# Performance work log

Hardware: AMD Instinct MI355X
Metric: run time of the kernel (lower is better)

## Reference

```python
import jax, jax.numpy as jnp
import numpy as np

N_NODES = 100000
N_EDGES = 1600000
N_GRAPHS = 64
NEG_SLOPE = 0.2


def gat_conv(x, W, att_src, att_dst, bias, edge_index, n_nodes, heads, out_ch, concat):
    """PyG-style GATConv (eval mode, self loops already included in edge_index)."""
    h = (x @ W).reshape(n_nodes, heads, out_ch)            # [N, H, C]
    a_src = jnp.einsum('nhc,hc->nh', h, att_src)           # [N, H]
    a_dst = jnp.einsum('nhc,hc->nh', h, att_dst)           # [N, H]
    src, dst = edge_index[0], edge_index[1]
    e = jax.nn.leaky_relu(a_src[src] + a_dst[dst], NEG_SLOPE)   # [E, H]
    # segment softmax over incoming edges of each destination node
    m = jax.ops.segment_max(e, dst, num_segments=n_nodes)      # [N, H]
    ex = jnp.exp(e - m[dst])
    denom = jax.ops.segment_sum(ex, dst, num_segments=n_nodes) # [N, H]
    alpha = ex / denom[dst]                                     # [E, H]
    msg = h[src] * alpha[:, :, None]                            # [E, H, C]
    out = jax.ops.segment_sum(msg, dst, num_segments=n_nodes)   # [N, H, C]
    if concat:
        out = out.reshape(n_nodes, heads * out_ch)
    else:
        out = out.mean(axis=1)
    return out + bias


def setup_inputs() -> dict:
    key = jax.random.key(0)
    ks = jax.random.split(key, 16)
    x = jax.random.normal(ks[0], (N_NODES, 1), dtype=jnp.float32)
    edge_index = jax.random.randint(ks[1], (2, N_EDGES), 0, N_NODES, dtype=jnp.int64)
    batch = jnp.sort(jax.random.randint(ks[2], (N_NODES,), 0, N_GRAPHS, dtype=jnp.int64))
    def glorot(k, shape):
        fan = (shape[0] + shape[-1])
        return jax.random.uniform(k, shape, jnp.float32, -1.0, 1.0) * np.sqrt(6.0 / fan)
    # layer 1: in=1, heads=8, out=8, concat
    W1 = glorot(ks[3], (1, 64))
    att_src1 = glorot(ks[4], (8, 8))
    att_dst1 = glorot(ks[5], (8, 8))
    b1 = jnp.zeros((64,), jnp.float32)
    # layer 2: in=64, heads=8, out=16, mean
    W2 = glorot(ks[6], (64, 128))
    att_src2 = glorot(ks[7], (8, 16))
    att_dst2 = glorot(ks[8], (8, 16))
    b2 = jnp.zeros((16,), jnp.float32)
    # fc 16 -> 4
    Wfc = glorot(ks[9], (16, 4))
    bfc = jnp.zeros((4,), jnp.float32)
    return dict(x=x, W1=W1, att_src1=att_src1, att_dst1=att_dst1, b1=b1,
                W2=W2, att_src2=att_src2, att_dst2=att_dst2, b2=b2,
                Wfc=Wfc, bfc=bfc, edge_index=edge_index, batch=batch)


def reference(x, W1, att_src1, att_dst1, b1, W2, att_src2, att_dst2, b2, Wfc, bfc, edge_index, batch):
    n = x.shape[0]
    # PyG GATConv default add_self_loops=True
    loops = jnp.arange(n, dtype=edge_index.dtype)
    ei = jnp.concatenate([edge_index, jnp.stack([loops, loops])], axis=1)
    h = gat_conv(x, W1, att_src1, att_dst1, b1, ei, n, heads=8, out_ch=8, concat=True)
    h = jax.nn.elu(h)
    # F.dropout(training=False) and attention dropout are no-ops in eval mode
    h = gat_conv(h, W2, att_src2, att_dst2, b2, ei, n, heads=8, out_ch=16, concat=False)
    # global mean pool over graphs
    sums = jax.ops.segment_sum(h, batch, num_segments=N_GRAPHS)          # [G, 16]
    cnts = jax.ops.segment_sum(jnp.ones((n,), h.dtype), batch, num_segments=N_GRAPHS)
    pooled = sums / jnp.maximum(cnts, 1.0)[:, None]
    return pooled @ Wfc + bfc                                            # [G, 4]
```

## Files before the change

### kernel.cpp

```cpp
#include <hip/hip_runtime.h>
#include <hip/hip_fp16.h>

#define N_NODES  100000
#define N_EDGES  1600000
#define N_GRAPHS 64

#define BINSH  9
#define NBIN   196
#define BINCAP 16384
#define EPB    4096

__device__ __forceinline__ float lrelu(float v) { return v > 0.f ? v : 0.2f * v; }
__device__ __forceinline__ float elu_f(float v) { return v > 0.f ? v : __expf(v) - 1.f; }
__device__ __forceinline__ float rdlane_f(float v, int lane) {
    return __int_as_float(__builtin_amdgcn_readlane(__float_as_int(v), lane));
}

__global__ __launch_bounds__(256) void k_binA(
    const int* __restrict__ src, const int* __restrict__ dst,
    const int* __restrict__ batch, int* __restrict__ gbin_cursor,
    int* __restrict__ cnt, int2* __restrict__ binned) {
    __shared__ int hist[NBIN], lexcl[NBIN], runbase[NBIN], lcur[NBIN];
    __shared__ int scan[256];
    __shared__ int gh[N_GRAPHS];
    __shared__ int2 stage[EPB];
    int t = threadIdx.x;
    int e0 = blockIdx.x * EPB;
    for (int b = t; b < NBIN; b += 256) hist[b] = 0;
    if (t < N_GRAPHS) gh[t] = 0;
    __syncthreads();
    int nid = blockIdx.x * 256 + t;
    if (nid < N_NODES) atomicAdd(&gh[batch[nid]], 1);
    for (int i = t; i < EPB; i += 256) {
        int e = e0 + i;
        if (e < N_EDGES) atomicAdd(&hist[dst[e] >> BINSH], 1);
    }
    __syncthreads();
    int v = (t < NBIN) ? hist[t] : 0;
    scan[t] = v;
    __syncthreads();
    for (int d = 1; d < 256; d <<= 1) {
        int a = (t >= d) ? scan[t - d] : 0;
        __syncthreads();
        scan[t] += a;
        __syncthreads();
    }
    if (t < NBIN) { lexcl[t] = scan[t] - v; lcur[t] = scan[t] - v; }
    __syncthreads();
    if (t < NBIN && hist[t] > 0) runbase[t] = atomicAdd(&gbin_cursor[t], hist[t]);
    if (t < N_GRAPHS && gh[t]) atomicAdd(&cnt[t], gh[t]);
    __syncthreads();
    for (int i = t; i < EPB; i += 256) {
        int e = e0 + i;
        if (e < N_EDGES) {
            int d = dst[e];
            int b = d >> BINSH;
            int p = atomicAdd(&lcur[b], 1);
            stage[p] = make_int2(src[e], d);
        }
    }
    __syncthreads();
    int m = N_EDGES - e0;
    if (m > EPB) m = EPB;
    for (int i = t; i < m; i += 256) {
        int2 pr = stage[i];
        int b = pr.y >> BINSH;
        binned[(size_t)b * BINCAP + runbase[b] + (i - lexcl[b])] = pr;
    }
}

__global__ void k_binscan(const int* __restrict__ gbin_cursor, int* __restrict__ bin_base) {
    __shared__ int sm[256];
    int t = threadIdx.x;
    int v = (t < NBIN) ? gbin_cursor[t] : 0;
    sm[t] = v;
    __syncthreads();
    for (int d = 1; d < 256; d <<= 1) {
        int a = (t >= d) ? sm[t - d] : 0;
        __syncthreads();
        sm[t] += a;
        __syncthreads();
    }
    if (t < NBIN) bin_base[t] = sm[t] - v;
    if (t == 0) bin_base[NBIN] = N_EDGES;
}

__global__ __launch_bounds__(1024) void k_binB(
    const int2* __restrict__ binned, const int* __restrict__ gbin_cursor,
    const int* __restrict__ bin_base, int* __restrict__ off, int* __restrict__ csr) {
    __shared__ int hist[512], sc[512];
    int b = blockIdx.x, t = threadIdx.x;
    int count = gbin_cursor[b];
    int ebase = bin_base[b];
    int node0 = b << BINSH;
    const int2* my = binned + (size_t)b * BINCAP;
    if (t < 512) hist[t] = 0;
    __syncthreads();
    for (int i = t; i < count; i += 1024) atomicAdd(&hist[my[i].y - node0], 1);
    __syncthreads();
    int v = (t < 512) ? hist[t] : 0;
    if (t < 512) sc[t] = v;
    __syncthreads();
    for (int d = 1; d < 512; d <<= 1) {
        int a = (t < 512 && t >= d) ? sc[t - d] : 0;
        __syncthreads();
        if (t < 512) sc[t] += a;
        __syncthreads();
    }
    if (t < 512) {
        int n = node0 + t;
        if (n < N_NODES) off[n] = ebase + sc[t] - v;
        hist[t] = sc[t] - v;
    }
    if (b == 0 && t == 0) off[N_NODES] = N_EDGES;
    __syncthreads();
    for (int i = t; i < count; i += 1024) {
        int2 pr = my[i];
        int p = atomicAdd(&hist[pr.y - node0], 1);
        csr[ebase + p] = pr.x;
    }
}

__global__ __launch_bounds__(256) void k_l1gemm(
    const float* __restrict__ x, const float* __restrict__ W1,
    const float* __restrict__ as1, const float* __restrict__ ad1,
    const float* __restrict__ b1, const float* __restrict__ W2,
    const float* __restrict__ as2, const float* __restrict__ ad2,
    const int* __restrict__ off, const int* __restrict__ csr,
    __half2* __restrict__ h2p, float2* __restrict__ ap, float2* __restrict__ dp) {
    __shared__ float4 smW4[32 * 64];
    __shared__ float smS1[16][8];
    __shared__ float smws[8], smwd[8];
    int t = threadIdx.x;
    for (int idx = t; idx < 2048; idx += 256) {
        int k2 = idx >> 6, ll = idx & 63;
        smW4[idx] = make_float4(W2[(2 * k2) * 128 + ll], W2[(2 * k2) * 128 + 64 + ll],
                                W2[(2 * k2 + 1) * 128 + ll], W2[(2 * k2 + 1) * 128 + 64 + ll]);
    }
    if (t < 8) {
        float s = 0.f, d = 0.f;
        for (int c = 0; c < 8; ++c) {
            float w = W1[t * 8 + c];
            s += w * as1[t * 8 + c];
            d += w * ad1[t * 8 + c];
        }
        smws[t] = s;
        smwd[t] = d;
    }
    __syncthreads();

    {
        int nl = t >> 4, c = t & 15;
        int n = blockIdx.x * 16 + nl;
        float ws[8], wd[8];
#pragma unroll
        for (int h = 0; h < 8; ++h) { ws[h] = smws[h]; wd[h] = smwd[h]; }
        float xn = x[n];
        float num[8], den[8];
#pragma unroll
        for (int h = 0; h < 8; ++h) { num[h] = 0.f; den[h] = 0.f; }
        if (c == 0) {
#pragma unroll
            for (int h = 0; h < 8; ++h) {
                float w = __expf(lrelu(xn * ws[h] + xn * wd[h]));
                den[h] = w;
                num[h] = w * xn;
            }
        }
        int b = off[n], e = off[n + 1];
        for (int i = b + c; i < e; i += 16) {
            int s = csr[i];
            float xs = x[s];
#pragma unroll
            for (int h = 0; h < 8; ++h) {
                float w = __expf(lrelu(xs * ws[h] + xn * wd[h]));
                den[h] += w;
                num[h] += w * xs;
            }
        }
#pragma unroll
        for (int d = 1; d < 16; d <<= 1) {
#pragma unroll
            for (int h = 0; h < 8; ++h) {
                num[h] += __shfl_xor(num[h], d, 64);
                den[h] += __shfl_xor(den[h], d, 64);
            }
        }
        if (c == 0) {
#pragma unroll
            for (int h = 0; h < 8; ++h) smS1[nl][h] = num[h] / den[h];
        }
    }
    __syncthreads();

    int wid = t >> 6, l = t & 63;
    float w1l = W1[l], b1l = b1[l];
    float asA = as2[l], asB = as2[64 + l], adA = ad2[l], adB = ad2[64 + l];
    for (int q = 0; q < 4; ++q) {
        int nl = wid * 4 + q;
        int n = blockIdx.x * 16 + nl;
        float a = elu_f(smS1[nl][l >> 3] * w1l + b1l);
        float acc0 = 0.f, acc1 = 0.f;
#pragma unroll
        for (int k2 = 0; k2 < 32; ++k2) {
            float4 wv = smW4[k2 * 64 + l];
            float a0 = rdlane_f(a, 2 * k2);
            float a1 = rdlane_f(a, 2 * k2 + 1);
            acc0 += a0 * wv.x + a1 * wv.z;
            acc1 += a0 * wv.y + a1 * wv.w;
        }
        h2p[n * 64 + l] = __floats2half2_rn(acc0, acc1);

        float pSA = acc0 * asA;
        float pSB = acc1 * asB;
        float pDA = acc0 * adA;
        float pDB = acc1 * adB;
#pragma unroll
        for (int d = 1; d < 16; d <<= 1) {
            pSA += __shfl_xor(pSA, d, 64);
            pSB += __shfl_xor(pSB, d, 64);
            pDA += __shfl_xor(pDA, d, 64);
            pDB += __shfl_xor(pDB, d, 64);
        }
        if ((l & 15) == 0) {
            int h = l >> 4;
            ap[n * 4 + h] = make_float2(pSA, pSB);
            dp[n * 4 + h] = make_float2(pDA, pDB);
        }
    }
}

__global__ __launch_bounds__(256) void k_layer2(
    const __half2* __restrict__ h2p, const float2* __restrict__ ap,
    const float2* __restrict__ dp, const int* __restrict__ off,
    const int* __restrict__ csr, const int* __restrict__ batch,
    float* __restrict__ pool) {
    __shared__ float smv[4][16];
    __shared__ int smg[4];
    const float* apf = (const float*)ap;
    const float* dpf = (const float*)dp;
    int t = threadIdx.x;
    int wid = t >> 6, l = t & 63;
    int n = blockIdx.x * 4 + wid;
    int hA = l >> 4;
    int hh = l & 7;
    int j8 = l >> 3;
    int fidx = 2 * (hh & 3) + (hh >> 2);
    float dn = dpf[n * 8 + fidx];

    float2 ad = dp[n * 4 + hA];
    float2 an = ap[n * 4 + hA];
    float wA = __expf(lrelu(an.x + ad.x));
    float wB = __expf(lrelu(an.y + ad.y));
    float2 hn = __half22float2(h2p[n * 64 + l]);
    float accA = wA * hn.x, accB = wB * hn.y;
    float denTA = wA, denTB = wB;
    float wsum = 0.f;

    int b = off[n];
    int deg = off[n + 1] - b;
    for (int base = 0; base < deg; base += 64) {
        int rem = deg - base;
        if (rem > 64) rem = 64;
        int sl = (l < rem) ? csr[b + base + l] : 0;
        int g = 0;
        for (; g + 8 <= rem; g += 8) {
            int sg = __shfl(sl, g + j8, 64);
            float w = __expf(lrelu(apf[sg * 8 + fidx] + dn));
            wsum += w;
#pragma unroll
            for (int j2 = 0; j2 < 8; ++j2) {
                int s = __builtin_amdgcn_readlane(sl, g + j2);
                float wa = __shfl(w, j2 * 8 + hA, 64);
                float wb = __shfl(w, j2 * 8 + hA + 4, 64);
                float2 gg = __half22float2(h2p[s * 64 + l]);
                accA = fmaf(wa, gg.x, accA);
                accB = fmaf(wb, gg.y, accB);
            }
        }
        if (g < rem) {
            int cnt = rem - g;
            int jj = (j8 < cnt) ? j8 : 0;
            int sg = __shfl(sl, g + jj, 64);
            float w = (j8 < cnt) ? __expf(lrelu(apf[sg * 8 + fidx] + dn)) : 0.f;
            wsum += w;
            for (int j2 = 0; j2 < cnt; ++j2) {
                int s = __builtin_amdgcn_readlane(sl, g + j2);
                float wa = __shfl(w, j2 * 8 + hA, 64);
                float wb = __shfl(w, j2 * 8 + hA + 4, 64);
                float2 gg = __half22float2(h2p[s * 64 + l]);
                accA = fmaf(wa, gg.x, accA);
                accB = fmaf(wb, gg.y, accB);
            }
        }
    }
    wsum += __shfl_xor(wsum, 8, 64);
    wsum += __shfl_xor(wsum, 16, 64);
    wsum += __shfl_xor(wsum, 32, 64);
    float denA = denTA + __shfl(wsum, hA, 64);
    float denB = denTB + __shfl(wsum, hA + 4, 64);

    float v = accA / denA + accB / denB;
    v += __shfl_xor(v, 16, 64);
    v += __shfl_xor(v, 32, 64);
    v *= 0.125f;
    if (l < 16) smv[wid][l] = v;
    if (l == 0) smg[wid] = batch[n];
    __syncthreads();
    if (t < 64) {
        int w = t >> 4, c = t & 15;
        int g = smg[w];
        bool leader = true;
        for (int w2 = 0; w2 < w; ++w2)
            if (smg[w2] == g) { leader = false; break; }
        if (leader) {
            float s = smv[w][c];
            for (int w2 = w + 1; w2 < 4; ++w2)
                if (smg[w2] == g) s += smv[w2][c];
            atomicAdd(&pool[g * 16 + c], s);
        }
    }
}

__global__ void k_final(const float* __restrict__ pool, const int* __restrict__ cnt,
                        const float* __restrict__ b2, const float* __restrict__ Wfc,
                        const float* __restrict__ bfc, float* __restrict__ out) {
    int t = threadIdx.x;
    int g = t >> 2, k = t & 3;
    float c = (float)(cnt[g] > 0 ? cnt[g] : 1);
    float acc = bfc[k];
#pragma unroll
    for (int ci = 0; ci < 16; ++ci)
        acc += (pool[g * 16 + ci] / c + b2[ci]) * Wfc[ci * 4 + k];
    out[g * 4 + k] = acc;
}

extern "C" void kernel_launch(void* const* d_in, const int* in_sizes, int n_in,
                              void* d_out, int out_size, void* d_ws, size_t ws_size,
                              hipStream_t stream) {
    const float* x   = (const float*)d_in[0];
    const float* W1  = (const float*)d_in[1];
    const float* as1 = (const float*)d_in[2];
    const float* ad1 = (const float*)d_in[3];
    const float* b1  = (const float*)d_in[4];
    const float* W2  = (const float*)d_in[5];
    const float* as2 = (const float*)d_in[6];
    const float* ad2 = (const float*)d_in[7];
    const float* b2  = (const float*)d_in[8];
    const float* Wfc = (const float*)d_in[9];
    const float* bfc = (const float*)d_in[10];
    const int* ei    = (const int*)d_in[11];
    const int* batch = (const int*)d_in[12];
    const int* srcv  = ei;
    const int* dstv  = ei + N_EDGES;

    char* ws = (char*)d_ws;
    size_t o = 0;
    auto alloc = [&](size_t bytes) {
        void* p = ws + o;
        o += (bytes + 255) & ~(size_t)255;
        return p;
    };
    int*    cnt     = (int*)alloc(64 * 4);
    float*  pool    = (float*)alloc(64 * 16 * 4);
    int*    gbin    = (int*)alloc(NBIN * 4);
    size_t  zbytes  = o;
    int*    bin_base= (int*)alloc((NBIN + 1) * 4);
    int*    off     = (int*)alloc((size_t)(N_NODES + 1) * 4);
    int*    csr     = (int*)alloc((size_t)N_EDGES * 4);
    char*   ubase   = (char*)alloc((size_t)N_NODES * 64 * 4 + (size_t)N_NODES * 4 * 8 * 2);
    int2*   binned  = (int2*)ubase;
    __half2* h2p    = (__half2*)ubase;
    float2* ap      = (float2*)(ubase + (size_t)N_NODES * 64 * 4);
    float2* dp      = (float2*)(ubase + (size_t)N_NODES * 64 * 4 + (size_t)N_NODES * 4 * 8);

    hipMemsetAsync(d_ws, 0, zbytes, stream);

    int nbA = (N_EDGES + EPB - 1) / EPB;

    k_binA<<<nbA, 256, 0, stream>>>(srcv, dstv, batch, gbin, cnt, binned);
    k_binscan<<<1, 256, 0, stream>>>(gbin, bin_base);
    k_binB<<<NBIN, 1024, 0, stream>>>(binned, gbin, bin_base, off, csr);
    k_l1gemm<<<N_NODES / 16, 256, 0, stream>>>(x, W1, as1, ad1, b1, W2, as2, ad2,
                                               off, csr, h2p, ap, dp);
    k_layer2<<<N_NODES / 4, 256, 0, stream>>>(h2p, ap, dp, off, csr, batch, pool);
    k_final<<<1, 256, 0, stream>>>(pool, cnt, b2, Wfc, bfc, (float*)d_out);
}
```

Before: 319.0 us.

## Split each layer-2 node's edge list across two wavefronts and merge via shared memory

The layer-2 aggregation kernel now assigns two wavefronts to each destination node. Each wave processes alternating 8-edge groups, and the partial accumulators and weight sums are combined through shared memory before normalization and pooling. This shortens each wave's serial gather chain and doubles the memory-level parallelism per node, which matters at an average degree of about 17. In exchange it adds a block barrier, shared-memory traffic, doubled grid size and duplicated per-node setup loads.

```diff
diff --git a/kernel.cpp b/kernel.cpp
--- a/kernel.cpp
+++ b/kernel.cpp
@@ -235,27 +235,35 @@
     const float2* __restrict__ dp, const int* __restrict__ off,
     const int* __restrict__ csr, const int* __restrict__ batch,
     float* __restrict__ pool) {
-    __shared__ float smv[4][16];
-    __shared__ int smg[4];
+    __shared__ float2 smacc[2][64];
+    __shared__ float smw[2][64];
+    __shared__ float smv[2][16];
+    __shared__ int smg[2];
     const float* apf = (const float*)ap;
     const float* dpf = (const float*)dp;
     int t = threadIdx.x;
     int wid = t >> 6, l = t & 63;
-    int n = blockIdx.x * 4 + wid;
+    int nl = wid >> 1, sub = wid & 1;
+    int n = blockIdx.x * 2 + nl;
     int hA = l >> 4;
     int hh = l & 7;
     int j8 = l >> 3;
     int fidx = 2 * (hh & 3) + (hh >> 2);
     float dn = dpf[n * 8 + fidx];
 
+    float accA = 0.f, accB = 0.f, wsum = 0.f;
+    float denTA = 0.f, denTB = 0.f;
     float2 ad = dp[n * 4 + hA];
-    float2 an = ap[n * 4 + hA];
-    float wA = __expf(lrelu(an.x + ad.x));
-    float wB = __expf(lrelu(an.y + ad.y));
-    float2 hn = __half22float2(h2p[n * 64 + l]);
-    float accA = wA * hn.x, accB = wB * hn.y;
-    float denTA = wA, denTB = wB;
-    float wsum = 0.f;
+    if (sub == 0) {
+        float2 an = ap[n * 4 + hA];
+        float wA = __expf(lrelu(an.x + ad.x));
+        float wB = __expf(lrelu(an.y + ad.y));
+        float2 hn = __half22float2(h2p[n * 64 + l]);
+        accA = wA * hn.x;
+        accB = wB * hn.y;
+        denTA = wA;
+        denTB = wB;
+    }
 
     int b = off[n];
     int deg = off[n + 1] - b;
@@ -263,60 +271,68 @@
         int rem = deg - base;
         if (rem > 64) rem = 64;
         int sl = (l < rem) ? csr[b + base + l] : 0;
-        int g = 0;
-        for (; g + 8 <= rem; g += 8) {
-            int sg = __shfl(sl, g + j8, 64);
-            float w = __expf(lrelu(apf[sg * 8 + fidx] + dn));
-            wsum += w;
-#pragma unroll
-            for (int j2 = 0; j2 < 8; ++j2) {
-                int s = __builtin_amdgcn_readlane(sl, g + j2);
-                float wa = __shfl(w, j2 * 8 + hA, 64);
-                float wb = __shfl(w, j2 * 8 + hA + 4, 64);
-                float2 gg = __half22float2(h2p[s * 64 + l]);
-                accA = fmaf(wa, gg.x, accA);
-                accB = fmaf(wb, gg.y, accB);
+        int ng = (rem + 7) >> 3;
+        for (int g8 = sub; g8 < ng; g8 += 2) {
+            int g = g8 * 8;
+            int cnt = rem - g;
+            if (cnt >= 8) {
+                int sg = __shfl(sl, g + j8, 64);
+                float w = __expf(lrelu(apf[sg * 8 + fidx] + dn));
+                wsum += w;
+#pragma unroll
+                for (int j2 = 0; j2 < 8; ++j2) {
+                    int s = __builtin_amdgcn_readlane(sl, g + j2);
+                    float wa = __shfl(w, j2 * 8 + hA, 64);
+                    float wb = __shfl(w, j2 * 8 + hA + 4, 64);
+                    float2 gg = __half22float2(h2p[s * 64 + l]);
+                    accA = fmaf(wa, gg.x, accA);
+                    accB = fmaf(wb, gg.y, accB);
+                }
+            } else {
+                int jj = (j8 < cnt) ? j8 : 0;
+                int sg = __shfl(sl, g + jj, 64);
+                float w = (j8 < cnt) ? __expf(lrelu(apf[sg * 8 + fidx] + dn)) : 0.f;
+                wsum += w;
+                for (int j2 = 0; j2 < cnt; ++j2) {
+                    int s = __builtin_amdgcn_readlane(sl, g + j2);
+                    float wa = __shfl(w, j2 * 8 + hA, 64);
+                    float wb = __shfl(w, j2 * 8 + hA + 4, 64);
+                    float2 gg = __half22float2(h2p[s * 64 + l]);
+                    accA = fmaf(wa, gg.x, accA);
+                    accB = fmaf(wb, gg.y, accB);
+                }
             }
         }
-        if (g < rem) {
-            int cnt = rem - g;
-            int jj = (j8 < cnt) ? j8 : 0;
-            int sg = __shfl(sl, g + jj, 64);
-            float w = (j8 < cnt) ? __expf(lrelu(apf[sg * 8 + fidx] + dn)) : 0.f;
-            wsum += w;
-            for (int j2 = 0; j2 < cnt; ++j2) {
-                int s = __builtin_amdgcn_readlane(sl, g + j2);
-                float wa = __shfl(w, j2 * 8 + hA, 64);
-                float wb = __shfl(w, j2 * 8 + hA + 4, 64);
-                float2 gg = __half22float2(h2p[s * 64 + l]);
-                accA = fmaf(wa, gg.x, accA);
-                accB = fmaf(wb, gg.y, accB);
-            }
-        }
-    }
-    wsum += __shfl_xor(wsum, 8, 64);
-    wsum += __shfl_xor(wsum, 16, 64);
-    wsum += __shfl_xor(wsum, 32, 64);
-    float denA = denTA + __shfl(wsum, hA, 64);
-    float denB = denTB + __shfl(wsum, hA + 4, 64);
-
-    float v = accA / denA + accB / denB;
-    v += __shfl_xor(v, 16, 64);
-    v += __shfl_xor(v, 32, 64);
-    v *= 0.125f;
-    if (l < 16) smv[wid][l] = v;
-    if (l == 0) smg[wid] = batch[n];
-    __syncthreads();
-    if (t < 64) {
+    }
+    if (sub == 1) {
+        smacc[nl][l] = make_float2(accA, accB);
+        smw[nl][l] = wsum;
+    }
+    __syncthreads();
+    if (sub == 0) {
+        float2 o = smacc[nl][l];
+        accA += o.x;
+        accB += o.y;
+        wsum += smw[nl][l];
+        wsum += __shfl_xor(wsum, 8, 64);
+        wsum += __shfl_xor(wsum, 16, 64);
+        wsum += __shfl_xor(wsum, 32, 64);
+        float denA = denTA + __shfl(wsum, hA, 64);
+        float denB = denTB + __shfl(wsum, hA + 4, 64);
+        float v = accA / denA + accB / denB;
+        v += __shfl_xor(v, 16, 64);
+        v += __shfl_xor(v, 32, 64);
+        v *= 0.125f;
+        if (l < 16) smv[nl][l] = v;
+        if (l == 0) smg[nl] = batch[n];
+    }
+    __syncthreads();
+    if (t < 32) {
         int w = t >> 4, c = t & 15;
         int g = smg[w];
-        bool leader = true;
-        for (int w2 = 0; w2 < w; ++w2)
-            if (smg[w2] == g) { leader = false; break; }
-        if (leader) {
+        if (w == 0 || smg[0] != g) {
             float s = smv[w][c];
-            for (int w2 = w + 1; w2 < 4; ++w2)
-                if (smg[w2] == g) s += smv[w2][c];
+            if (w == 0 && smg[1] == g) s += smv[1][c];
             atomicAdd(&pool[g * 16 + c], s);
         }
     }
@@ -383,6 +399,6 @@
     k_binB<<<NBIN, 1024, 0, stream>>>(binned, gbin, bin_base, off, csr);
     k_l1gemm<<<N_NODES / 16, 256, 0, stream>>>(x, W1, as1, ad1, b1, W2, as2, ad2,
                                                off, csr, h2p, ap, dp);
-    k_layer2<<<N_NODES / 4, 256, 0, stream>>>(h2p, ap, dp, off, csr, batch, pool);
+    k_layer2<<<N_NODES / 2, 256, 0, stream>>>(h2p, ap, dp, off, csr, batch, pool);
     k_final<<<1, 256, 0, stream>>>(pool, cnt, b2, Wfc, bfc, (float*)d_out);
 }
```

Result: slower. 372.3 us (+16.7%).

## Use finer CSR bins, 32 nodes per layer-1 block, 16-wide layer-2 gather

Applied to the files above, without the earlier changes.

The CSR binning is halved in granularity: 256-node bins, 2048 edges per block and 512-thread binning blocks, so binB does smaller scans and binA launches more blocks. The layer-1 fused kernel now handles 32 nodes per block instead of 16, so the shared-memory staging of W2 is paid over twice as many nodes. Layer-2 aggregation gains a 16-neighbor unrolled path that issues all 16 half2 row loads before doing the FMAs, exposing more memory-level parallelism. The cost is more registers and less parallelism per block in layer 1, which may hurt occupancy.

```diff
diff --git a/kernel.cpp b/kernel.cpp
--- a/kernel.cpp
+++ b/kernel.cpp
@@ -5,10 +5,10 @@
 #define N_EDGES  1600000
 #define N_GRAPHS 64
 
-#define BINSH  9
-#define NBIN   196
-#define BINCAP 16384
-#define EPB    4096
+#define BINSH  8
+#define NBIN   392
+#define BINCAP 8192
+#define EPB    2048
 
 __device__ __forceinline__ float lrelu(float v) { return v > 0.f ? v : 0.2f * v; }
 __device__ __forceinline__ float elu_f(float v) { return v > 0.f ? v : __expf(v) - 1.f; }
@@ -16,22 +16,22 @@
     return __int_as_float(__builtin_amdgcn_readlane(__float_as_int(v), lane));
 }
 
-__global__ __launch_bounds__(256) void k_binA(
+__global__ __launch_bounds__(512) void k_binA(
     const int* __restrict__ src, const int* __restrict__ dst,
     const int* __restrict__ batch, int* __restrict__ gbin_cursor,
     int* __restrict__ cnt, int2* __restrict__ binned) {
     __shared__ int hist[NBIN], lexcl[NBIN], runbase[NBIN], lcur[NBIN];
-    __shared__ int scan[256];
+    __shared__ int scan[512];
     __shared__ int gh[N_GRAPHS];
     __shared__ int2 stage[EPB];
     int t = threadIdx.x;
     int e0 = blockIdx.x * EPB;
-    for (int b = t; b < NBIN; b += 256) hist[b] = 0;
+    for (int b = t; b < NBIN; b += 512) hist[b] = 0;
     if (t < N_GRAPHS) gh[t] = 0;
     __syncthreads();
-    int nid = blockIdx.x * 256 + t;
+    int nid = blockIdx.x * 512 + t;
     if (nid < N_NODES) atomicAdd(&gh[batch[nid]], 1);
-    for (int i = t; i < EPB; i += 256) {
+    for (int i = t; i < EPB; i += 512) {
         int e = e0 + i;
         if (e < N_EDGES) atomicAdd(&hist[dst[e] >> BINSH], 1);
     }
@@ -39,7 +39,7 @@
     int v = (t < NBIN) ? hist[t] : 0;
     scan[t] = v;
     __syncthreads();
-    for (int d = 1; d < 256; d <<= 1) {
+    for (int d = 1; d < 512; d <<= 1) {
         int a = (t >= d) ? scan[t - d] : 0;
         __syncthreads();
         scan[t] += a;
@@ -50,7 +50,7 @@
     if (t < NBIN && hist[t] > 0) runbase[t] = atomicAdd(&gbin_cursor[t], hist[t]);
     if (t < N_GRAPHS && gh[t]) atomicAdd(&cnt[t], gh[t]);
     __syncthreads();
-    for (int i = t; i < EPB; i += 256) {
+    for (int i = t; i < EPB; i += 512) {
         int e = e0 + i;
         if (e < N_EDGES) {
             int d = dst[e];
@@ -62,7 +62,7 @@
     __syncthreads();
     int m = N_EDGES - e0;
     if (m > EPB) m = EPB;
-    for (int i = t; i < m; i += 256) {
+    for (int i = t; i < m; i += 512) {
         int2 pr = stage[i];
         int b = pr.y >> BINSH;
         binned[(size_t)b * BINCAP + runbase[b] + (i - lexcl[b])] = pr;
@@ -70,12 +70,12 @@
 }
 
 __global__ void k_binscan(const int* __restrict__ gbin_cursor, int* __restrict__ bin_base) {
-    __shared__ int sm[256];
+    __shared__ int sm[512];
     int t = threadIdx.x;
     int v = (t < NBIN) ? gbin_cursor[t] : 0;
     sm[t] = v;
     __syncthreads();
-    for (int d = 1; d < 256; d <<= 1) {
+    for (int d = 1; d < 512; d <<= 1) {
         int a = (t >= d) ? sm[t - d] : 0;
         __syncthreads();
         sm[t] += a;
@@ -88,26 +88,26 @@
 __global__ __launch_bounds__(1024) void k_binB(
     const int2* __restrict__ binned, const int* __restrict__ gbin_cursor,
     const int* __restrict__ bin_base, int* __restrict__ off, int* __restrict__ csr) {
-    __shared__ int hist[512], sc[512];
+    __shared__ int hist[256], sc[256];
     int b = blockIdx.x, t = threadIdx.x;
     int count = gbin_cursor[b];
     int ebase = bin_base[b];
     int node0 = b << BINSH;
     const int2* my = binned + (size_t)b * BINCAP;
-    if (t < 512) hist[t] = 0;
+    if (t < 256) hist[t] = 0;
     __syncthreads();
     for (int i = t; i < count; i += 1024) atomicAdd(&hist[my[i].y - node0], 1);
     __syncthreads();
-    int v = (t < 512) ? hist[t] : 0;
-    if (t < 512) sc[t] = v;
-    __syncthreads();
-    for (int d = 1; d < 512; d <<= 1) {
-        int a = (t < 512 && t >= d) ? sc[t - d] : 0;
-        __syncthreads();
-        if (t < 512) sc[t] += a;
-        __syncthreads();
-    }
-    if (t < 512) {
+    int v = (t < 256) ? hist[t] : 0;
+    if (t < 256) sc[t] = v;
+    __syncthreads();
+    for (int d = 1; d < 256; d <<= 1) {
+        int a = (t < 256 && t >= d) ? sc[t - d] : 0;
+        __syncthreads();
+        if (t < 256) sc[t] += a;
+        __syncthreads();
+    }
+    if (t < 256) {
         int n = node0 + t;
         if (n < N_NODES) off[n] = ebase + sc[t] - v;
         hist[t] = sc[t] - v;
@@ -129,7 +129,7 @@
     const int* __restrict__ off, const int* __restrict__ csr,
     __half2* __restrict__ h2p, float2* __restrict__ ap, float2* __restrict__ dp) {
     __shared__ float4 smW4[32 * 64];
-    __shared__ float smS1[16][8];
+    __shared__ float smS1[32][8];
     __shared__ float smws[8], smwd[8];
     int t = threadIdx.x;
     for (int idx = t; idx < 2048; idx += 256) {
@@ -150,45 +150,48 @@
     __syncthreads();
 
     {
-        int nl = t >> 4, c = t & 15;
-        int n = blockIdx.x * 16 + nl;
+        int c = t & 15;
         float ws[8], wd[8];
 #pragma unroll
         for (int h = 0; h < 8; ++h) { ws[h] = smws[h]; wd[h] = smwd[h]; }
-        float xn = x[n];
-        float num[8], den[8];
-#pragma unroll
-        for (int h = 0; h < 8; ++h) { num[h] = 0.f; den[h] = 0.f; }
-        if (c == 0) {
-#pragma unroll
-            for (int h = 0; h < 8; ++h) {
-                float w = __expf(lrelu(xn * ws[h] + xn * wd[h]));
-                den[h] = w;
-                num[h] = w * xn;
-            }
-        }
-        int b = off[n], e = off[n + 1];
-        for (int i = b + c; i < e; i += 16) {
-            int s = csr[i];
-            float xs = x[s];
-#pragma unroll
-            for (int h = 0; h < 8; ++h) {
-                float w = __expf(lrelu(xs * ws[h] + xn * wd[h]));
-                den[h] += w;
-                num[h] += w * xs;
-            }
-        }
-#pragma unroll
-        for (int d = 1; d < 16; d <<= 1) {
-#pragma unroll
-            for (int h = 0; h < 8; ++h) {
-                num[h] += __shfl_xor(num[h], d, 64);
-                den[h] += __shfl_xor(den[h], d, 64);
-            }
-        }
-        if (c == 0) {
-#pragma unroll
-            for (int h = 0; h < 8; ++h) smS1[nl][h] = num[h] / den[h];
+        for (int p = 0; p < 2; ++p) {
+            int nl = p * 16 + (t >> 4);
+            int n = blockIdx.x * 32 + nl;
+            float xn = x[n];
+            float num[8], den[8];
+#pragma unroll
+            for (int h = 0; h < 8; ++h) { num[h] = 0.f; den[h] = 0.f; }
+            if (c == 0) {
+#pragma unroll
+                for (int h = 0; h < 8; ++h) {
+                    float w = __expf(lrelu(xn * ws[h] + xn * wd[h]));
+                    den[h] = w;
+                    num[h] = w * xn;
+                }
+            }
+            int bo = off[n], e = off[n + 1];
+            for (int i = bo + c; i < e; i += 16) {
+                int s = csr[i];
+                float xs = x[s];
+#pragma unroll
+                for (int h = 0; h < 8; ++h) {
+                    float w = __expf(lrelu(xs * ws[h] + xn * wd[h]));
+                    den[h] += w;
+                    num[h] += w * xs;
+                }
+            }
+#pragma unroll
+            for (int d = 1; d < 16; d <<= 1) {
+#pragma unroll
+                for (int h = 0; h < 8; ++h) {
+                    num[h] += __shfl_xor(num[h], d, 64);
+                    den[h] += __shfl_xor(den[h], d, 64);
+                }
+            }
+            if (c == 0) {
+#pragma unroll
+                for (int h = 0; h < 8; ++h) smS1[nl][h] = num[h] / den[h];
+            }
         }
     }
     __syncthreads();
@@ -196,9 +199,9 @@
     int wid = t >> 6, l = t & 63;
     float w1l = W1[l], b1l = b1[l];
     float asA = as2[l], asB = as2[64 + l], adA = ad2[l], adB = ad2[64 + l];
-    for (int q = 0; q < 4; ++q) {
-        int nl = wid * 4 + q;
-        int n = blockIdx.x * 16 + nl;
+    for (int q = 0; q < 8; ++q) {
+        int nl = wid * 8 + q;
+        int n = blockIdx.x * 32 + nl;
         float a = elu_f(smS1[nl][l >> 3] * w1l + b1l);
         float acc0 = 0.f, acc1 = 0.f;
 #pragma unroll
@@ -264,6 +267,35 @@
         if (rem > 64) rem = 64;
         int sl = (l < rem) ? csr[b + base + l] : 0;
         int g = 0;
+        for (; g + 16 <= rem; g += 16) {
+            int sgA = __shfl(sl, g + j8, 64);
+            int sgB = __shfl(sl, g + 8 + j8, 64);
+            float wg0 = __expf(lrelu(apf[sgA * 8 + fidx] + dn));
+            float wg1 = __expf(lrelu(apf[sgB * 8 + fidx] + dn));
+            wsum += wg0 + wg1;
+            __half2 hv[16];
+#pragma unroll
+            for (int k = 0; k < 16; ++k) {
+                int s = __builtin_amdgcn_readlane(sl, g + k);
+                hv[k] = h2p[s * 64 + l];
+            }
+#pragma unroll
+            for (int k = 0; k < 8; ++k) {
+                float wa = __shfl(wg0, k * 8 + hA, 64);
+                float wb = __shfl(wg0, k * 8 + hA + 4, 64);
+                float2 gg = __half22float2(hv[k]);
+                accA = fmaf(wa, gg.x, accA);
+                accB = fmaf(wb, gg.y, accB);
+            }
+#pragma unroll
+            for (int k = 0; k < 8; ++k) {
+                float wa = __shfl(wg1, k * 8 + hA, 64);
+                float wb = __shfl(wg1, k * 8 + hA + 4, 64);
+                float2 gg = __half22float2(hv[8 + k]);
+                accA = fmaf(wa, gg.x, accA);
+                accB = fmaf(wb, gg.y, accB);
+            }
+        }
         for (; g + 8 <= rem; g += 8) {
             int sg = __shfl(sl, g + j8, 64);
             float w = __expf(lrelu(apf[sg * 8 + fidx] + dn));
@@ -378,10 +410,10 @@
 
     int nbA = (N_EDGES + EPB - 1) / EPB;
 
-    k_binA<<<nbA, 256, 0, stream>>>(srcv, dstv, batch, gbin, cnt, binned);
-    k_binscan<<<1, 256, 0, stream>>>(gbin, bin_base);
+    k_binA<<<nbA, 512, 0, stream>>>(srcv, dstv, batch, gbin, cnt, binned);
+    k_binscan<<<1, 512, 0, stream>>>(gbin, bin_base);
     k_binB<<<NBIN, 1024, 0, stream>>>(binned, gbin, bin_base, off, csr);
-    k_l1gemm<<<N_NODES / 16, 256, 0, stream>>>(x, W1, as1, ad1, b1, W2, as2, ad2,
+    k_l1gemm<<<N_NODES / 32, 256, 0, stream>>>(x, W1, as1, ad1, b1, W2, as2, ad2,
                                                off, csr, h2p, ap, dp);
     k_layer2<<<N_NODES / 4, 256, 0, stream>>>(h2p, ap, dp, off, csr, batch, pool);
     k_final<<<1, 256, 0, stream>>>(pool, cnt, b2, Wfc, bfc, (float*)d_out);
```

After: 352.2 us. 1.1x slower.
